# Optimization experiments

Measured on AMD Instinct MI355X. Metric: run time of the kernel, lower is better.

The kernel has to match this reference:

```python
import jax, jax.numpy as jnp
import numpy as np

H = 16  # num_heads
EPS = 1e-5


def _ln(x, g, b):
    m = x.mean(-1, keepdims=True)
    v = x.var(-1, keepdims=True)
    return (x - m) / jnp.sqrt(v + EPS) * g + b


def _heads(x):
    b, s, d = x.shape
    return x.reshape(b, s, H, d // H).transpose(0, 2, 1, 3)  # [B,H,S,dh]


def _merge_buggy(z):
    # replicate torch view([B,H,S,dh] -> [B,S,H*dh]) WITHOUT head transpose
    b, h, s, dh = z.shape
    return z.reshape(b, s, h * dh)


def _attn(q_in, kv_in, resid, wq, bq, wk, bk, wv, bv, g, be, scale_by_seq, apply_triu):
    q = _heads(q_in @ wq + bq)
    k = _heads(kv_in @ wk + bk)
    v = _heads(kv_in @ wv + bv)
    qk = jnp.einsum('bhqd,bhkd->bhqk', q, k)
    qk = jnp.where(jnp.isnan(qk), -jnp.inf, qk)
    if scale_by_seq:
        qk = qk / jnp.sqrt(jnp.asarray(qk.shape[-1], qk.dtype))  # sqrt(seq_len), as in source
    a = jax.nn.softmax(qk, axis=-1)
    a = jnp.where(jnp.isnan(a), 0.0, a)
    v = jnp.where(jnp.isnan(v), 0.0, v)
    if apply_triu:
        s = a.shape[-1]
        a = a * jnp.triu(jnp.ones((s, s), a.dtype))  # post-softmax multiplicative mask
    z = jnp.einsum('bhqk,bhkd->bhqd', a, v)
    z = _merge_buggy(z)
    return _ln(resid + z, g, be)


def setup_inputs() -> dict:
    key = jax.random.key(0)
    ks = jax.random.split(key, 20)
    B, S, D, F = 2, 2048, 1024, 1024
    p = lambda k, sh: (jax.random.normal(k, sh, jnp.float32) * 0.02)
    inp = {
        'encoded': jax.random.normal(ks[0], (B, S, D), jnp.float32),
        'decoded': jax.random.normal(ks[1], (B, S, D), jnp.float32),
        'sa_wq': p(ks[2], (D, D)), 'sa_bq': jnp.zeros((D,), jnp.float32),
        'sa_wk': p(ks[3], (D, D)), 'sa_bk': jnp.zeros((D,), jnp.float32),
        'sa_wv': p(ks[4], (D, D)), 'sa_bv': jnp.zeros((D,), jnp.float32),
        'sa_g': jnp.ones((D,), jnp.float32), 'sa_b': jnp.zeros((D,), jnp.float32),
        'ca_wq': p(ks[5], (D, D)), 'ca_bq': jnp.zeros((D,), jnp.float32),
        'ca_wk': p(ks[6], (D, D)), 'ca_bk': jnp.zeros((D,), jnp.float32),
        'ca_wv': p(ks[7], (D, D)), 'ca_bv': jnp.zeros((D,), jnp.float32),
        'ca_g': jnp.ones((D,), jnp.float32), 'ca_b': jnp.zeros((D,), jnp.float32),
        'ffn_w1': p(ks[8], (D, F)), 'ffn_b1': jnp.zeros((F,), jnp.float32),
        'ffn_w2': p(ks[9], (F, D)), 'ffn_b2': jnp.zeros((D,), jnp.float32),
        'ffn_g': jnp.ones((D,), jnp.float32), 'ffn_b': jnp.zeros((D,), jnp.float32),
    }
    return inp


def reference(encoded, decoded,
              sa_wq, sa_bq, sa_wk, sa_bk, sa_wv, sa_bv, sa_g, sa_b,
              ca_wq, ca_bq, ca_wk, ca_bk, ca_wv, ca_bv, ca_g, ca_b,
              ffn_w1, ffn_b1, ffn_w2, ffn_b2, ffn_g, ffn_b):
    # masked self-attention (quirky: scale by sqrt(S), post-softmax triu mask)
    x = _attn(decoded, decoded, decoded, sa_wq, sa_bq, sa_wk, sa_bk, sa_wv, sa_bv,
              sa_g, sa_b, scale_by_seq=True, apply_triu=True)
    # cross-attention (no scale, no mask)
    x = _attn(x, encoded, x, ca_wq, ca_bq, ca_wk, ca_bk, ca_wv, ca_bv,
              ca_g, ca_b, scale_by_seq=False, apply_triu=False)
    # FFN with residual + LayerNorm (dropout = identity in eval)
    y = jax.nn.relu(x @ ffn_w1 + ffn_b1) @ ffn_w2 + ffn_b2
    return _ln(y + x, ffn_g, ffn_b)
```

## Files before the change

### kernel.cpp

```cpp
#include <hip/hip_runtime.h>
#include <hip/hip_bf16.h>
#include <cstdint>


typedef __attribute__((ext_vector_type(8))) short bf16x8;
typedef __attribute__((ext_vector_type(4))) float f32x4;
typedef unsigned short u16;

#define MFMA16(a, b, c) __builtin_amdgcn_mfma_f32_16x16x32_bf16((a), (b), (c), 0, 0, 0)

__device__ __forceinline__ u16 f2b(float f) {
    __hip_bfloat16 h = __float2bfloat16(f);
    return __builtin_bit_cast(u16, h);
}
__device__ __forceinline__ float b2f(u16 u) {
    return __builtin_bit_cast(float, (uint32_t)u << 16);
}
__device__ __forceinline__ void g2lds16(const u16* g, u16* l) {
    __builtin_amdgcn_global_load_lds((const __attribute__((address_space(1))) void*)g,
                                     (__attribute__((address_space(3))) void*)l, 16, 0, 0);
}

__global__ __launch_bounds__(256) void cast_bf16_kernel(const float* __restrict__ x,
                                                        u16* __restrict__ y, int n4) {
    int i = blockIdx.x * 256 + threadIdx.x;
    if (i >= n4) return;
    float4 v = reinterpret_cast<const float4*>(x)[i];
    ushort4 o;
    o.x = f2b(v.x); o.y = f2b(v.y); o.z = f2b(v.z); o.w = f2b(v.w);
    reinterpret_cast<ushort4*>(y)[i] = o;
}

__global__ __launch_bounds__(256) void wcast_all_kernel(
    const float* __restrict__ w0, const float* __restrict__ w1,
    const float* __restrict__ w2, const float* __restrict__ w3,
    const float* __restrict__ w4, const float* __restrict__ w5,
    const float* __restrict__ w6, const float* __restrict__ w7,
    u16* __restrict__ wt) {
    __shared__ float t[32][33];
    const float* W;
    switch (blockIdx.z) {
        case 0: W = w0; break; case 1: W = w1; break;
        case 2: W = w2; break; case 3: W = w3; break;
        case 4: W = w4; break; case 5: W = w5; break;
        case 6: W = w6; break; default: W = w7; break;
    }
    u16* Wt = wt + (size_t)blockIdx.z * 1048576;
    int tx = threadIdx.x & 31, ty = threadIdx.x >> 5;
    int bx = blockIdx.x * 32, by = blockIdx.y * 32;
#pragma unroll
    for (int j = 0; j < 4; ++j)
        t[ty + j * 8][tx] = W[(size_t)(by + ty + j * 8) * 1024 + bx + tx];
    __syncthreads();
#pragma unroll
    for (int j = 0; j < 4; ++j)
        Wt[(size_t)(bx + ty + j * 8) * 1024 + by + tx] = f2b(t[tx][ty + j * 8]);
}

__global__ __launch_bounds__(256) void vtrans_kernel(const u16* __restrict__ V,
                                                     u16* __restrict__ Vt) {
    __shared__ u16 t[32][34];
    const int tx = threadIdx.x & 31, ty = threadIdx.x >> 5;
    const int s0 = blockIdx.x * 32, d0 = blockIdx.y * 32, b = blockIdx.z;
    const u16* src = V + (size_t)b * 2048 * 1024;
    u16* dst = Vt + (size_t)b * 1024 * 2048;
#pragma unroll
    for (int j = 0; j < 4; ++j)
        t[ty + j * 8][tx] = src[(size_t)(s0 + ty + j * 8) * 1024 + d0 + tx];
    __syncthreads();
#pragma unroll
    for (int j = 0; j < 4; ++j)
        dst[(size_t)(d0 + ty + j * 8) * 2048 + s0 + tx] = t[tx][ty + j * 8];
}

__global__ __launch_bounds__(256) void gemm_kernel(
    const u16* __restrict__ A0, const u16* __restrict__ A1,
    const u16* __restrict__ Btb,
    const float* __restrict__ bias0, const float* __restrict__ bias1,
    const float* __restrict__ bias2,
    u16* __restrict__ o0, u16* __restrict__ o1, u16* __restrict__ o2,
    int relu, float oscale0) {
    const int K = 1024;
    __shared__ __align__(16) u16 As[2][128][32];
    __shared__ __align__(16) u16 Bs[2][128][32];
    const int tid = threadIdx.x, lane = tid & 63, w = tid >> 6;
    const int wm = w >> 1, wn = w & 1, l15 = lane & 15, l4 = lane >> 4;
    const int bm = blockIdx.y * 128, bn = blockIdx.x * 128;
    const int which = bn >> 10;
    const u16* A = (which == 0) ? A0 : A1;
    const int srow = lane >> 2, sc = lane & 3;
    const int scs = (sc ^ (srow & 3)) * 8;
    const u16* aW = A + (size_t)(bm + w * 16 + srow) * K + scs;
    const u16* bW = Btb + (size_t)(bn + w * 16 + srow) * K + scs;
    f32x4 acc[4][4] = {};

#define GSTAGE(bf, kt)                                                  \
    do {                                                                \
        g2lds16(aW + (kt), &As[bf][w * 16][0]);                         \
        g2lds16(aW + (size_t)64 * K + (kt), &As[bf][64 + w * 16][0]);   \
        g2lds16(bW + (kt), &Bs[bf][w * 16][0]);                         \
        g2lds16(bW + (size_t)64 * K + (kt), &Bs[bf][64 + w * 16][0]);   \
    } while (0)

    const int nt = K / 32;
    GSTAGE(0, 0);
    for (int t = 0; t < nt; ++t) {
        __syncthreads();
        if (t + 1 < nt) GSTAGE((t + 1) & 1, (t + 1) * 32);
        const int bf = t & 1;
        bf16x8 af[4], bfr[4];
#pragma unroll
        for (int m = 0; m < 4; ++m) {
            int row = wm * 64 + m * 16 + l15;
            af[m] = *reinterpret_cast<const bf16x8*>(&As[bf][row][(l4 ^ (l15 & 3)) * 8]);
        }
#pragma unroll
        for (int n = 0; n < 4; ++n) {
            int row = wn * 64 + n * 16 + l15;
            bfr[n] = *reinterpret_cast<const bf16x8*>(&Bs[bf][row][(l4 ^ (l15 & 3)) * 8]);
        }
        __builtin_amdgcn_s_setprio(1);
#pragma unroll
        for (int m = 0; m < 4; ++m)
#pragma unroll
            for (int n = 0; n < 4; ++n)
                acc[m][n] = MFMA16(af[m], bfr[n], acc[m][n]);
        __builtin_amdgcn_s_setprio(0);
    }
#undef GSTAGE
    const float* bias = which == 0 ? bias0 : (which == 1 ? bias1 : bias2);
    u16* outp = which == 0 ? o0 : (which == 1 ? o1 : o2);
    const float osc = which == 0 ? oscale0 : 1.0f;
    const int bnl = bn & 1023;
#pragma unroll
    for (int m = 0; m < 4; ++m) {
#pragma unroll
        for (int n = 0; n < 4; ++n) {
            int col = bnl + wn * 64 + n * 16 + l15;
            float bv = bias[col];
            int row0 = bm + wm * 64 + m * 16 + l4 * 4;
#pragma unroll
            for (int r = 0; r < 4; ++r) {
                float v = (acc[m][n][r] + bv) * osc;
                if (relu) v = fmaxf(v, 0.f);
                outp[(size_t)(row0 + r) * 1024 + col] = f2b(v);
            }
        }
    }
}

template <int CAUSAL>
__global__ __launch_bounds__(256) void attn_kernel(const u16* __restrict__ Qb,
                                                   const u16* __restrict__ Kb,
                                                   const u16* __restrict__ Vt,
                                                   u16* __restrict__ Z) {
    const int S = 2048, D = 1024;
    __shared__ __align__(16) u16 Ks[2][64][64];
    __shared__ __align__(16) u16 Vs[2][64][64];
    __shared__ __align__(16) u16 Ps[4][16][72];
    const int tid = threadIdx.x, lane = tid & 63, w = tid >> 6;
    const int l15 = lane & 15, l4 = lane >> 4;
    const int hwid = blockIdx.x;
    const int wkid = (hwid & 7) * 128 + (hwid >> 3);
    const int qb = wkid & 31, h = (wkid >> 5) & 15, b = wkid >> 9;
    const int q0 = qb * 64 + w * 16;
    const int qg = q0 + l15;
    const size_t baseQ = (size_t)b * S * D + h * 64;
    const size_t baseVt = ((size_t)(b * 16 + h) * 64) * 2048;

    bf16x8 aq0, aq1;
    {
        const u16* qp = Qb + baseQ + (size_t)qg * D + l4 * 8;
        aq0 = *reinterpret_cast<const bf16x8*>(qp);
        aq1 = *reinterpret_cast<const bf16x8*>(qp + 32);
    }
    float lrp0 = 0.f, lrp1 = 0.f, lrp2 = 0.f, lrp3 = 0.f;
    f32x4 Oacc[4] = {};

    const int swzA = (l4 ^ (l15 & 7)) * 8;
    const int swzB = ((l4 + 4) ^ (l15 & 7)) * 8;
    const u16* ksbA = &Ks[0][l15][swzA];
    const u16* ksbB = &Ks[0][l15][swzB];
    const u16* vsbA = &Vs[0][l15][swzA];
    const u16* vsbB = &Vs[0][l15][swzB];
    u16* pswb = &Ps[w][l15][l4 * 4];
    const u16* psrb = &Ps[w][l15][l4 * 8];

    const int srow = lane >> 3, sc8 = lane & 7;
    const int scs = (sc8 ^ srow) * 8;
    const u16* kWn0 = Kb + baseQ + (size_t)(srow + (w * 2 + 0) * 8) * D + scs;
    const u16* kWn1 = Kb + baseQ + (size_t)(srow + (w * 2 + 1) * 8) * D + scs;
    const u16* vWn0 = Vt + baseVt + (size_t)(srow + (w * 2 + 0) * 8) * 2048 + scs;
    const u16* vWn1 = Vt + baseVt + (size_t)(srow + (w * 2 + 1) * 8) * 2048 + scs;

    const int NT = S / 64;
    const int t0pv = CAUSAL ? qb : 0;

    g2lds16(kWn0, &Ks[0][(w * 2 + 0) * 8][0]);
    g2lds16(kWn1, &Ks[0][(w * 2 + 1) * 8][0]);
    kWn0 += 64 * D; kWn1 += 64 * D;
    if (0 >= t0pv) {
        g2lds16(vWn0, &Vs[0][(w * 2 + 0) * 8][0]);
        g2lds16(vWn1, &Vs[0][(w * 2 + 1) * 8][0]);
    }
    vWn0 += 64; vWn1 += 64;

    int tcur = 0;
#define ATILE(B)                                                               \
    do {                                                                       \
        __syncthreads();                                                       \
        if (tcur + 1 < NT) {                                                   \
            g2lds16(kWn0, &Ks[(B) ^ 1][(w * 2 + 0) * 8][0]);                   \
            g2lds16(kWn1, &Ks[(B) ^ 1][(w * 2 + 1) * 8][0]);                   \
            if (tcur + 1 >= t0pv) {                                            \
                g2lds16(vWn0, &Vs[(B) ^ 1][(w * 2 + 0) * 8][0]);               \
                g2lds16(vWn1, &Vs[(B) ^ 1][(w * 2 + 1) * 8][0]);               \
            }                                                                  \
        }                                                                      \
        kWn0 += 64 * D; kWn1 += 64 * D; vWn0 += 64; vWn1 += 64;                \
        const bool dopv = (tcur >= t0pv);                                      \
        const bool maskT = CAUSAL && (tcur == qb);                             \
        bf16x8 vf[2][4];                                                       \
        if (dopv) {                                                            \
            _Pragma("unroll")                                                  \
            for (int n = 0; n < 4; ++n) {                                      \
                vf[0][n] = *reinterpret_cast<const bf16x8*>(                   \
                    vsbA + (B) * 4096 + n * 1024);                             \
                vf[1][n] = *reinterpret_cast<const bf16x8*>(                   \
                    vsbB + (B) * 4096 + n * 1024);                             \
            }                                                                  \
        }                                                                      \
        const f32x4 zero = {0.f, 0.f, 0.f, 0.f};                               \
        _Pragma("unroll")                                                      \
        for (int kg = 0; kg < 4; ++kg) {                                       \
            bf16x8 k0 = *reinterpret_cast<const bf16x8*>(                      \
                ksbA + (B) * 4096 + kg * 1024);                                \
            bf16x8 k1 = *reinterpret_cast<const bf16x8*>(                      \
                ksbB + (B) * 4096 + kg * 1024);                                \
            f32x4 sv = MFMA16(k0, aq0, zero);                                  \
            sv = MFMA16(k1, aq1, sv);                                          \
            float e0 = __builtin_exp2f(sv[0]);                                 \
            float e1 = __builtin_exp2f(sv[1]);                                 \
            float e2 = __builtin_exp2f(sv[2]);                                 \
            float e3 = __builtin_exp2f(sv[3]);                                 \
            lrp0 += e0; lrp1 += e1; lrp2 += e2; lrp3 += e3;                    \
            if (dopv) {                                                        \
                if (maskT) {                                                   \
                    int key = tcur * 64 + kg * 16 + l4 * 4;                    \
                    if (key + 0 < qg) e0 = 0.f;                                \
                    if (key + 1 < qg) e1 = 0.f;                                \
                    if (key + 2 < qg) e2 = 0.f;                                \
                    if (key + 3 < qg) e3 = 0.f;                                \
                }                                                              \
                ushort4 pw;                                                    \
                pw.x = f2b(e0); pw.y = f2b(e1);                                \
                pw.z = f2b(e2); pw.w = f2b(e3);                                \
                *reinterpret_cast<ushort4*>(pswb + kg * 16) = pw;              \
            }                                                                  \
        }                                                                      \
        if (dopv) {                                                            \
            asm volatile("s_waitcnt lgkmcnt(0)" ::: "memory");                 \
            __builtin_amdgcn_sched_barrier(0);                                 \
            __builtin_amdgcn_s_setprio(1);                                     \
            _Pragma("unroll")                                                  \
            for (int kh = 0; kh < 2; ++kh) {                                   \
                bf16x8 pa = *reinterpret_cast<const bf16x8*>(psrb + kh * 32);  \
                _Pragma("unroll")                                              \
                for (int n = 0; n < 4; ++n)                                    \
                    Oacc[n] = MFMA16(vf[kh][n], pa, Oacc[n]);                  \
            }                                                                  \
            __builtin_amdgcn_s_setprio(0);                                     \
        }                                                                      \
        ++tcur;                                                                \
    } while (0)

    for (int i = 0; i < NT / 2; ++i) {
        ATILE(0);
        ATILE(1);
    }
#undef ATILE

    float lr = (lrp0 + lrp1) + (lrp2 + lrp3);
    lr += __shfl_xor(lr, 16);
    lr += __shfl_xor(lr, 32);

    {
        float inv = 1.f / lr;
        int orow = h * 128 + (qg >> 4);
        int oc0 = (qg & 15) * 64;
#pragma unroll
        for (int n = 0; n < 4; ++n) {
            ushort4 o;
            o.x = f2b(Oacc[n][0] * inv); o.y = f2b(Oacc[n][1] * inv);
            o.z = f2b(Oacc[n][2] * inv); o.w = f2b(Oacc[n][3] * inv);
            *reinterpret_cast<ushort4*>(
                &Z[(size_t)b * S * D + (size_t)orow * D + oc0 + n * 16 + l4 * 4]) = o;
        }
    }
}

__global__ __launch_bounds__(256) void add_ln_kernel(const float* __restrict__ resid,
                                                     const u16* __restrict__ zb,
                                                     const float* __restrict__ g,
                                                     const float* __restrict__ bb,
                                                     float* __restrict__ outF,
                                                     u16* __restrict__ outH) {
    const int row = blockIdx.x * 4 + (threadIdx.x >> 6);
    const int lane = threadIdx.x & 63;
    const float* rp = resid + (size_t)row * 1024;
    const u16* zp = zb + (size_t)row * 1024;
    float v[16];
    float s = 0.f, s2 = 0.f;
#pragma unroll
    for (int k = 0; k < 4; ++k) {
        int col = k * 256 + lane * 4;
        float4 rv = *reinterpret_cast<const float4*>(rp + col);
        ushort4 zv = *reinterpret_cast<const ushort4*>(zp + col);
        float x0 = rv.x + b2f(zv.x);
        float x1 = rv.y + b2f(zv.y);
        float x2 = rv.z + b2f(zv.z);
        float x3 = rv.w + b2f(zv.w);
        v[k * 4 + 0] = x0; v[k * 4 + 1] = x1; v[k * 4 + 2] = x2; v[k * 4 + 3] = x3;
        s += x0 + x1 + x2 + x3;
        s2 += x0 * x0 + x1 * x1 + x2 * x2 + x3 * x3;
    }
#pragma unroll
    for (int o = 32; o >= 1; o >>= 1) {
        s += __shfl_xor(s, o);
        s2 += __shfl_xor(s2, o);
    }
    float mean = s * (1.f / 1024.f);
    float var = s2 * (1.f / 1024.f) - mean * mean;
    float rstd = rsqrtf(var + 1e-5f);
#pragma unroll
    for (int k = 0; k < 4; ++k) {
        int col = k * 256 + lane * 4;
        float4 gv = *reinterpret_cast<const float4*>(g + col);
        float4 bv = *reinterpret_cast<const float4*>(bb + col);
        float o0 = (v[k * 4 + 0] - mean) * rstd * gv.x + bv.x;
        float o1 = (v[k * 4 + 1] - mean) * rstd * gv.y + bv.y;
        float o2 = (v[k * 4 + 2] - mean) * rstd * gv.z + bv.z;
        float o3 = (v[k * 4 + 3] - mean) * rstd * gv.w + bv.w;
        if (outF) {
            float4 o = make_float4(o0, o1, o2, o3);
            *reinterpret_cast<float4*>(outF + (size_t)row * 1024 + col) = o;
        }
        if (outH) {
            ushort4 o;
            o.x = f2b(o0); o.y = f2b(o1); o.z = f2b(o2); o.w = f2b(o3);
            *reinterpret_cast<ushort4*>(outH + (size_t)row * 1024 + col) = o;
        }
    }
}

extern "C" void kernel_launch(void* const* d_in, const int* in_sizes, int n_in,
                              void* d_out, int out_size, void* d_ws, size_t ws_size,
                              hipStream_t stream) {
    const float* enc   = (const float*)d_in[0];
    const float* dec   = (const float*)d_in[1];
    const float* sa_wq = (const float*)d_in[2];  const float* sa_bq = (const float*)d_in[3];
    const float* sa_wk = (const float*)d_in[4];  const float* sa_bk = (const float*)d_in[5];
    const float* sa_wv = (const float*)d_in[6];  const float* sa_bv = (const float*)d_in[7];
    const float* sa_g  = (const float*)d_in[8];  const float* sa_b  = (const float*)d_in[9];
    const float* ca_wq = (const float*)d_in[10]; const float* ca_bq = (const float*)d_in[11];
    const float* ca_wk = (const float*)d_in[12]; const float* ca_bk = (const float*)d_in[13];
    const float* ca_wv = (const float*)d_in[14]; const float* ca_bv = (const float*)d_in[15];
    const float* ca_g  = (const float*)d_in[16]; const float* ca_b  = (const float*)d_in[17];
    const float* w1    = (const float*)d_in[18]; const float* b1    = (const float*)d_in[19];
    const float* w2    = (const float*)d_in[20]; const float* b2    = (const float*)d_in[21];
    const float* fg    = (const float*)d_in[22]; const float* fb    = (const float*)d_in[23];
    float* out = (float*)d_out;

    const size_t WSZ = 1048576;
    const size_t ASZ = 4194304;

    u16* wt   = (u16*)d_ws;
    u16* decB = wt + 8 * WSZ;
    u16* encB = decB + ASZ;
    u16* qB   = encB + ASZ;
    u16* kB   = qB + ASZ;
    u16* vB   = kB + ASZ;
    u16* zB   = vB + ASZ;
    float* x1f = (float*)(zB + ASZ);
    u16* xb   = (u16*)(x1f + ASZ);

    const float Q_SCALE_SELF = 0.031879354f;
    const float Q_SCALE_CROSS = 1.4426950408889634f;

    wcast_all_kernel<<<dim3(32, 32, 8), 256, 0, stream>>>(sa_wq, sa_wk, sa_wv, ca_wq,
                                                          ca_wk, ca_wv, w1, w2, wt);
    cast_bf16_kernel<<<4096, 256, 0, stream>>>(dec, decB, (int)(ASZ / 4));
    cast_bf16_kernel<<<4096, 256, 0, stream>>>(enc, encB, (int)(ASZ / 4));

    gemm_kernel<<<dim3(24, 32), 256, 0, stream>>>(decB, decB, wt,
                                                  sa_bq, sa_bk, sa_bv, qB, kB, vB,
                                                  0, Q_SCALE_SELF);
    vtrans_kernel<<<dim3(64, 32, 2), 256, 0, stream>>>(vB, xb);
    attn_kernel<1><<<1024, 256, 0, stream>>>(qB, kB, xb, zB);
    add_ln_kernel<<<1024, 256, 0, stream>>>(dec, zB, sa_g, sa_b, x1f, xb);

    gemm_kernel<<<dim3(24, 32), 256, 0, stream>>>(xb, encB, wt + 3 * WSZ,
                                                  ca_bq, ca_bk, ca_bv, qB, kB, vB,
                                                  0, Q_SCALE_CROSS);
    vtrans_kernel<<<dim3(64, 32, 2), 256, 0, stream>>>(vB, xb);
    attn_kernel<0><<<1024, 256, 0, stream>>>(qB, kB, xb, zB);
    add_ln_kernel<<<1024, 256, 0, stream>>>(x1f, zB, ca_g, ca_b, x1f, xb);

    gemm_kernel<<<dim3(8, 32), 256, 0, stream>>>(xb, xb, wt + 6 * WSZ,
                                                 b1, b1, b1, qB, qB, qB, 1, 1.0f);
    gemm_kernel<<<dim3(8, 32), 256, 0, stream>>>(qB, qB, wt + 7 * WSZ,
                                                 b2, b2, b2, zB, zB, zB, 0, 1.0f);
    add_ln_kernel<<<1024, 256, 0, stream>>>(x1f, zB, fg, fb, out, nullptr);
}
```

Measured before the change: 339.9 us.

## Process two query sub-tiles per wave in attention; remap GEMM block order

```diff
diff --git a/kernel.cpp b/kernel.cpp
--- a/kernel.cpp
+++ b/kernel.cpp
@@ -85,7 +85,11 @@
     __shared__ __align__(16) u16 Bs[2][128][32];
     const int tid = threadIdx.x, lane = tid & 63, w = tid >> 6;
     const int wm = w >> 1, wn = w & 1, l15 = lane & 15, l4 = lane >> 4;
-    const int bm = blockIdx.y * 128, bn = blockIdx.x * 128;
+    const int nx = gridDim.x;
+    const int fhw = blockIdx.y * nx + blockIdx.x;
+    const int cpx = (nx * 32) >> 3;
+    const int lid = (fhw & 7) * cpx + (fhw >> 3);
+    const int bm = (lid & 31) * 128, bn = (lid >> 5) * 128;
     const int which = bn >> 10;
     const u16* A = (which == 0) ? A0 : A1;
     const int srow = lane >> 2, sc = lane & 3;
@@ -157,25 +161,28 @@
     const int S = 2048, D = 1024;
     __shared__ __align__(16) u16 Ks[2][64][64];
     __shared__ __align__(16) u16 Vs[2][64][64];
-    __shared__ __align__(16) u16 Ps[4][16][72];
+    __shared__ __align__(16) u16 Ps[4][32][72];
     const int tid = threadIdx.x, lane = tid & 63, w = tid >> 6;
     const int l15 = lane & 15, l4 = lane >> 4;
     const int hwid = blockIdx.x;
-    const int wkid = (hwid & 7) * 128 + (hwid >> 3);
-    const int qb = wkid & 31, h = (wkid >> 5) & 15, b = wkid >> 9;
-    const int q0 = qb * 64 + w * 16;
+    const int wkid = (hwid & 7) * 64 + (hwid >> 3);
+    const int qb = wkid & 15, h = (wkid >> 4) & 15, b = wkid >> 8;
+    const int q0 = qb * 128 + w * 32;
     const int qg = q0 + l15;
     const size_t baseQ = (size_t)b * S * D + h * 64;
     const size_t baseVt = ((size_t)(b * 16 + h) * 64) * 2048;
 
-    bf16x8 aq0, aq1;
+    bf16x8 aq00, aq10, aq01, aq11;
     {
         const u16* qp = Qb + baseQ + (size_t)qg * D + l4 * 8;
-        aq0 = *reinterpret_cast<const bf16x8*>(qp);
-        aq1 = *reinterpret_cast<const bf16x8*>(qp + 32);
-    }
-    float lrp0 = 0.f, lrp1 = 0.f, lrp2 = 0.f, lrp3 = 0.f;
-    f32x4 Oacc[4] = {};
+        aq00 = *reinterpret_cast<const bf16x8*>(qp);
+        aq10 = *reinterpret_cast<const bf16x8*>(qp + 32);
+        aq01 = *reinterpret_cast<const bf16x8*>(qp + 16 * D);
+        aq11 = *reinterpret_cast<const bf16x8*>(qp + 16 * D + 32);
+    }
+    float la0 = 0.f, la1 = 0.f, la2 = 0.f, la3 = 0.f;
+    float lb0 = 0.f, lb1 = 0.f, lb2 = 0.f, lb3 = 0.f;
+    f32x4 O0[4] = {}, O1[4] = {};
 
     const int swzA = (l4 ^ (l15 & 7)) * 8;
     const int swzB = ((l4 + 4) ^ (l15 & 7)) * 8;
@@ -183,8 +190,10 @@
     const u16* ksbB = &Ks[0][l15][swzB];
     const u16* vsbA = &Vs[0][l15][swzA];
     const u16* vsbB = &Vs[0][l15][swzB];
-    u16* pswb = &Ps[w][l15][l4 * 4];
-    const u16* psrb = &Ps[w][l15][l4 * 8];
+    u16* pswb0 = &Ps[w][l15][l4 * 4];
+    u16* pswb1 = &Ps[w][16 + l15][l4 * 4];
+    const u16* psrb0 = &Ps[w][l15][l4 * 8];
+    const u16* psrb1 = &Ps[w][16 + l15][l4 * 8];
 
     const int srow = lane >> 3, sc8 = lane & 7;
     const int scs = (sc8 ^ srow) * 8;
@@ -194,7 +203,7 @@
     const u16* vWn1 = Vt + baseVt + (size_t)(srow + (w * 2 + 1) * 8) * 2048 + scs;
 
     const int NT = S / 64;
-    const int t0pv = CAUSAL ? qb : 0;
+    const int t0pv = CAUSAL ? (qb * 2) : 0;
 
     g2lds16(kWn0, &Ks[0][(w * 2 + 0) * 8][0]);
     g2lds16(kWn1, &Ks[0][(w * 2 + 1) * 8][0]);
@@ -219,7 +228,7 @@
         }                                                                      \
         kWn0 += 64 * D; kWn1 += 64 * D; vWn0 += 64; vWn1 += 64;                \
         const bool dopv = (tcur >= t0pv);                                      \
-        const bool maskT = CAUSAL && (tcur == qb);                             \
+        const bool maskT = CAUSAL && dopv && (tcur * 64 < q0 + 32);            \
         bf16x8 vf[2][4];                                                       \
         if (dopv) {                                                            \
             _Pragma("unroll")                                                  \
@@ -237,25 +246,39 @@
                 ksbA + (B) * 4096 + kg * 1024);                                \
             bf16x8 k1 = *reinterpret_cast<const bf16x8*>(                      \
                 ksbB + (B) * 4096 + kg * 1024);                                \
-            f32x4 sv = MFMA16(k0, aq0, zero);                                  \
-            sv = MFMA16(k1, aq1, sv);                                          \
-            float e0 = __builtin_exp2f(sv[0]);                                 \
-            float e1 = __builtin_exp2f(sv[1]);                                 \
-            float e2 = __builtin_exp2f(sv[2]);                                 \
-            float e3 = __builtin_exp2f(sv[3]);                                 \
-            lrp0 += e0; lrp1 += e1; lrp2 += e2; lrp3 += e3;                    \
+            f32x4 sv0 = MFMA16(k0, aq00, zero);                                \
+            sv0 = MFMA16(k1, aq10, sv0);                                       \
+            f32x4 sv1 = MFMA16(k0, aq01, zero);                                \
+            sv1 = MFMA16(k1, aq11, sv1);                                       \
+            float e00 = __builtin_exp2f(sv0[0]);                               \
+            float e01 = __builtin_exp2f(sv0[1]);                               \
+            float e02 = __builtin_exp2f(sv0[2]);                               \
+            float e03 = __builtin_exp2f(sv0[3]);                               \
+            float e10 = __builtin_exp2f(sv1[0]);                               \
+            float e11 = __builtin_exp2f(sv1[1]);                               \
+            float e12 = __builtin_exp2f(sv1[2]);                               \
+            float e13 = __builtin_exp2f(sv1[3]);                               \
+            la0 += e00; la1 += e01; la2 += e02; la3 += e03;                    \
+            lb0 += e10; lb1 += e11; lb2 += e12; lb3 += e13;                    \
             if (dopv) {                                                        \
                 if (maskT) {                                                   \
                     int key = tcur * 64 + kg * 16 + l4 * 4;                    \
-                    if (key + 0 < qg) e0 = 0.f;                                \
-                    if (key + 1 < qg) e1 = 0.f;                                \
-                    if (key + 2 < qg) e2 = 0.f;                                \
-                    if (key + 3 < qg) e3 = 0.f;                                \
+                    if (key + 0 < qg) e00 = 0.f;                               \
+                    if (key + 1 < qg) e01 = 0.f;                               \
+                    if (key + 2 < qg) e02 = 0.f;                               \
+                    if (key + 3 < qg) e03 = 0.f;                               \
+                    if (key + 0 < qg + 16) e10 = 0.f;                          \
+                    if (key + 1 < qg + 16) e11 = 0.f;                          \
+                    if (key + 2 < qg + 16) e12 = 0.f;                          \
+                    if (key + 3 < qg + 16) e13 = 0.f;                          \
                 }                                                              \
-                ushort4 pw;                                                    \
-                pw.x = f2b(e0); pw.y = f2b(e1);                                \
-                pw.z = f2b(e2); pw.w = f2b(e3);                                \
-                *reinterpret_cast<ushort4*>(pswb + kg * 16) = pw;              \
+                ushort4 pw0, pw1;                                              \
+                pw0.x = f2b(e00); pw0.y = f2b(e01);                            \
+                pw0.z = f2b(e02); pw0.w = f2b(e03);                            \
+                pw1.x = f2b(e10); pw1.y = f2b(e11);                            \
+                pw1.z = f2b(e12); pw1.w = f2b(e13);                            \
+                *reinterpret_cast<ushort4*>(pswb0 + kg * 16) = pw0;            \
+                *reinterpret_cast<ushort4*>(pswb1 + kg * 16) = pw1;            \
             }                                                                  \
         }                                                                      \
         if (dopv) {                                                            \
@@ -264,10 +287,13 @@
             __builtin_amdgcn_s_setprio(1);                                     \
             _Pragma("unroll")                                                  \
             for (int kh = 0; kh < 2; ++kh) {                                   \
-                bf16x8 pa = *reinterpret_cast<const bf16x8*>(psrb + kh * 32);  \
+                bf16x8 pa0 = *reinterpret_cast<const bf16x8*>(psrb0 + kh * 32);\
+                bf16x8 pa1 = *reinterpret_cast<const bf16x8*>(psrb1 + kh * 32);\
                 _Pragma("unroll")                                              \
-                for (int n = 0; n < 4; ++n)                                    \
-                    Oacc[n] = MFMA16(vf[kh][n], pa, Oacc[n]);                  \
+                for (int n = 0; n < 4; ++n) {                                  \
+                    O0[n] = MFMA16(vf[kh][n], pa0, O0[n]);                     \
+                    O1[n] = MFMA16(vf[kh][n], pa1, O1[n]);                     \
+                }                                                              \
             }                                                                  \
             __builtin_amdgcn_s_setprio(0);                                     \
         }                                                                      \
@@ -280,21 +306,28 @@
     }
 #undef ATILE
 
-    float lr = (lrp0 + lrp1) + (lrp2 + lrp3);
-    lr += __shfl_xor(lr, 16);
-    lr += __shfl_xor(lr, 32);
+    float lr0 = (la0 + la1) + (la2 + la3);
+    lr0 += __shfl_xor(lr0, 16);
+    lr0 += __shfl_xor(lr0, 32);
+    float lr1 = (lb0 + lb1) + (lb2 + lb3);
+    lr1 += __shfl_xor(lr1, 16);
+    lr1 += __shfl_xor(lr1, 32);
 
     {
-        float inv = 1.f / lr;
+        float inv0 = 1.f / lr0, inv1 = 1.f / lr1;
         int orow = h * 128 + (qg >> 4);
         int oc0 = (qg & 15) * 64;
+        size_t zb0 = (size_t)b * S * D + (size_t)orow * D + oc0;
+        size_t zb1 = zb0 + D;
 #pragma unroll
         for (int n = 0; n < 4; ++n) {
-            ushort4 o;
-            o.x = f2b(Oacc[n][0] * inv); o.y = f2b(Oacc[n][1] * inv);
-            o.z = f2b(Oacc[n][2] * inv); o.w = f2b(Oacc[n][3] * inv);
-            *reinterpret_cast<ushort4*>(
-                &Z[(size_t)b * S * D + (size_t)orow * D + oc0 + n * 16 + l4 * 4]) = o;
+            ushort4 o0v, o1v;
+            o0v.x = f2b(O0[n][0] * inv0); o0v.y = f2b(O0[n][1] * inv0);
+            o0v.z = f2b(O0[n][2] * inv0); o0v.w = f2b(O0[n][3] * inv0);
+            o1v.x = f2b(O1[n][0] * inv1); o1v.y = f2b(O1[n][1] * inv1);
+            o1v.z = f2b(O1[n][2] * inv1); o1v.w = f2b(O1[n][3] * inv1);
+            *reinterpret_cast<ushort4*>(&Z[zb0 + n * 16 + l4 * 4]) = o0v;
+            *reinterpret_cast<ushort4*>(&Z[zb1 + n * 16 + l4 * 4]) = o1v;
         }
     }
 }
@@ -396,14 +429,14 @@
                                                   sa_bq, sa_bk, sa_bv, qB, kB, vB,
                                                   0, Q_SCALE_SELF);
     vtrans_kernel<<<dim3(64, 32, 2), 256, 0, stream>>>(vB, xb);
-    attn_kernel<1><<<1024, 256, 0, stream>>>(qB, kB, xb, zB);
+    attn_kernel<1><<<512, 256, 0, stream>>>(qB, kB, xb, zB);
     add_ln_kernel<<<1024, 256, 0, stream>>>(dec, zB, sa_g, sa_b, x1f, xb);
 
     gemm_kernel<<<dim3(24, 32), 256, 0, stream>>>(xb, encB, wt + 3 * WSZ,
                                                   ca_bq, ca_bk, ca_bv, qB, kB, vB,
                                                   0, Q_SCALE_CROSS);
     vtrans_kernel<<<dim3(64, 32, 2), 256, 0, stream>>>(vB, xb);
-    attn_kernel<0><<<1024, 256, 0, stream>>>(qB, kB, xb, zB);
+    attn_kernel<0><<<512, 256, 0, stream>>>(qB, kB, xb, zB);
     add_ln_kernel<<<1024, 256, 0, stream>>>(x1f, zB, ca_g, ca_b, x1f, xb);
 
     gemm_kernel<<<dim3(8, 32), 256, 0, stream>>>(xb, xb, wt + 6 * WSZ,
```

Measured after the change: 344.4 us. About the same (+1.3%).
